# Kernel tuning notes

Measured on AMD Instinct MI355X. Metric: run time of the kernel, lower is better.

The kernel has to match this reference:

```python
import jax, jax.numpy as jnp
import numpy as np

NUM_HEADS = 8
HEAD_DIM = 64
EPS = 1e-4

def _act(x):
    # 1 + elu(x) == where(x > 0, x + 1, exp(x))
    return jnp.where(x > 0, x + 1.0, jnp.exp(x))

def setup_inputs() -> dict:
    key = jax.random.key(0)
    k1, k2, k3 = jax.random.split(key, 3)
    b, n, dim = 16, 4096, 512
    inner = NUM_HEADS * HEAD_DIM
    x = jax.random.normal(k1, (b, n, dim), dtype=jnp.float32)
    W_qkv = jax.random.normal(k2, (3 * inner, dim), dtype=jnp.float32) * (dim ** -0.5)
    W_out = jax.random.normal(k3, (dim, inner), dtype=jnp.float32) * (inner ** -0.5)
    b_out = jnp.zeros((dim,), dtype=jnp.float32)
    return {"x": x, "W_qkv": W_qkv, "W_out": W_out, "b_out": b_out}

def reference(x, W_qkv, W_out, b_out):
    b, n, dim = x.shape
    inner = NUM_HEADS * HEAD_DIM
    qkv = x @ W_qkv.T                                     # [b, n, 3*inner]
    q, k, v = jnp.split(qkv, 3, axis=-1)
    def to_heads(t):
        return t.reshape(b, n, NUM_HEADS, HEAD_DIM).transpose(0, 2, 1, 3)  # [b, h, n, d]
    q, k, v = to_heads(q), to_heads(k), to_heads(v)
    q = _act(q)
    k = _act(k)
    # kv = sum_n k_n (outer) v_n  -> [b, h, d, e]
    kv = jnp.einsum('bhnd,bhne->bhde', k, v)
    # denominator: q . sum_n k_n, clamped at eps
    k_sum = k.sum(axis=-2)                                # [b, h, d]
    z = 1.0 / jnp.maximum(jnp.einsum('bhnd,bhd->bhn', q, k_sum), EPS)
    out = jnp.einsum('bhnd,bhde,bhn->bhne', q, kv, z)     # [b, h, n, e]
    out = out.transpose(0, 2, 1, 3).reshape(b, n, inner)  # [b, n, h*d]
    return out @ W_out.T + b_out
```

## Files before the change

kernel.cpp:

```cpp
#include <hip/hip_runtime.h>


typedef unsigned short u16;
typedef u16 u16x4 __attribute__((ext_vector_type(4)));
typedef u16 u16x8 __attribute__((ext_vector_type(8)));
typedef __bf16 bf16x8 __attribute__((ext_vector_type(8)));
typedef float f32x4 __attribute__((ext_vector_type(4)));

__device__ __forceinline__ float bf2f(u16 x) {
    union { unsigned u; float f; } t; t.u = ((unsigned)x) << 16; return t.f;
}
__device__ __forceinline__ u16 f2bf(float f) {
    union { float f; unsigned u; } t; t.f = f;
    unsigned r = t.u + 0x7fffu + ((t.u >> 16) & 1u);
    return (u16)(r >> 16);
}
__device__ __forceinline__ float act_fn(float v) {
    return v > 0.0f ? v + 1.0f : __expf(v);
}
__device__ __forceinline__ void cvt8(const float* __restrict__ s, u16* __restrict__ d) {
    f32x4 lo = *(const f32x4*)s;
    f32x4 hi = *(const f32x4*)(s + 4);
    u16x8 o = { f2bf(lo[0]), f2bf(lo[1]), f2bf(lo[2]), f2bf(lo[3]),
                f2bf(hi[0]), f2bf(hi[1]), f2bf(hi[2]), f2bf(hi[3]) };
    *(u16x8*)d = o;
}
__device__ __forceinline__ void gld16(const u16* g, u16* l) {
    __builtin_amdgcn_global_load_lds(
        (__attribute__((address_space(1))) const void*)g,
        (__attribute__((address_space(3))) void*)l, 16, 0, 0);
}

__global__ __launch_bounds__(256) void convert_all(const float* __restrict__ x,
                                                   const float* __restrict__ Wqkv,
                                                   const float* __restrict__ Wout,
                                                   u16* __restrict__ xb,
                                                   u16* __restrict__ wq,
                                                   u16* __restrict__ wo,
                                                   float* __restrict__ kvg)
{
    size_t u = (size_t)blockIdx.x * 256 + threadIdx.x;
    if (u < 4194304ull) {
        cvt8(x + u * 8, xb + u * 8);
    } else if (u < 4292608ull) {
        u -= 4194304ull;
        const int drow = (int)(u >> 6);
        int srow;
        if (drow < 512) srow = drow;
        else {
            const int t = drow - 512, h = t >> 7, j = t & 127;
            srow = (j < 64) ? (512 + h * 64 + j) : (1024 + h * 64 + (j - 64));
        }
        cvt8(Wqkv + (size_t)srow * 512 + (u & 63) * 8, wq + u * 8);
    } else if (u < 4325376ull) {
        u -= 4292608ull; cvt8(Wout + u * 8, wo + u * 8);
    } else {
        u -= 4325376ull;
        f32x4 z = { 0.f, 0.f, 0.f, 0.f };
        *(f32x4*)&kvg[u * 8] = z;
        *(f32x4*)&kvg[u * 8 + 4] = z;
    }
}

__global__ __launch_bounds__(512, 4) void gemm_qkv(const u16* __restrict__ A,
                                                   const u16* __restrict__ Bw,
                                                   u16* __restrict__ Cq,
                                                   float* __restrict__ kvglob)
{
    __shared__ u16 SMF[16384];
    const int nt = blockIdx.x;
    const int mt = blockIdx.y;
    const size_t row0 = (size_t)mt * 128;
    const int col0 = nt * 128;
    const int tid = threadIdx.x, wave = tid >> 6, lane = tid & 63;
    const int frow = lane & 15, quad = lane >> 4;
    const int wr = (wave >> 1) * 32, wc = (wave & 1) * 64;

    f32x4 acc[2][4] = {};

    const int r0 = tid >> 2, c0 = (tid & 3) * 8;
    const u16* gA0 = A + (row0 + r0) * 512 + c0;
    const u16* gB0 = Bw + (size_t)(col0 + r0) * 512 + c0;

#define QKV_STAGE(buf, k0) do {                                   \
        u16* As_ = SMF + (buf) * 8192;                            \
        u16* Bs_ = As_ + 4096;                                    \
        gld16(gA0 + (k0), As_ + wave * 512);                      \
        gld16(gB0 + (k0), Bs_ + wave * 512);                      \
    } while (0)

    QKV_STAGE(0, 0);
    __syncthreads();
    int cur = 0;
    for (int t = 0; t < 16; ++t) {
        if (t < 15) QKV_STAGE(cur ^ 1, (t + 1) * 32);
        const u16* As_ = SMF + cur * 8192;
        const u16* Bs_ = As_ + 4096;
        bf16x8 af[2], bfr[4];
#pragma unroll
        for (int mi = 0; mi < 2; ++mi)
            af[mi] = *(const bf16x8*)&As_[(wr + mi * 16 + frow) * 32 + quad * 8];
#pragma unroll
        for (int ni = 0; ni < 4; ++ni)
            bfr[ni] = *(const bf16x8*)&Bs_[(wc + ni * 16 + frow) * 32 + quad * 8];
#pragma unroll
        for (int mi = 0; mi < 2; ++mi)
#pragma unroll
            for (int ni = 0; ni < 4; ++ni)
                acc[mi][ni] = __builtin_amdgcn_mfma_f32_16x16x32_bf16(af[mi], bfr[ni], acc[mi][ni], 0, 0, 0);
        __syncthreads();
        cur ^= 1;
    }
#undef QKV_STAGE

    if (col0 < 512) {
#pragma unroll
        for (int mi = 0; mi < 2; ++mi) {
#pragma unroll
            for (int ni = 0; ni < 4; ++ni) {
                const int c = col0 + wc + ni * 16 + frow;
                const size_t rbase = row0 + wr + mi * 16 + quad * 4;
#pragma unroll
                for (int reg = 0; reg < 4; ++reg)
                    Cq[(rbase + reg) * 512 + c] = f2bf(act_fn(acc[mi][ni][reg]));
            }
        }
        return;
    }

    u16* KT = SMF;
    u16* VT = SMF + 4608;
    for (int i = tid; i < 16 * 72; i += 512)
        VT[64 * 72 + i] = (i < 64) ? (u16)0x3F80 : (u16)0;

    const bool is_k = (wc == 0);
    f32x4 kvacc[5] = {};

#pragma unroll
    for (int half = 0; half < 2; ++half) {
        __syncthreads();
        if ((wave >> 2) == half) {
#pragma unroll
            for (int mi = 0; mi < 2; ++mi) {
                const int n0 = wr + mi * 16 + quad * 4 - half * 64;
#pragma unroll
                for (int ni = 0; ni < 4; ++ni) {
                    const int cl = wc + ni * 16 + frow;
                    u16x4 o2;
#pragma unroll
                    for (int reg = 0; reg < 4; ++reg) {
                        float v = acc[mi][ni][reg];
                        if (is_k) v = act_fn(v);
                        o2[reg] = f2bf(v);
                    }
                    if (is_k) *(u16x4*)&KT[cl * 72 + n0] = o2;
                    else      *(u16x4*)&VT[(cl - 64) * 72 + n0] = o2;
                }
            }
        }
        __syncthreads();
        if (wave < 4) {
#pragma unroll
            for (int c = 0; c < 2; ++c) {
                bf16x8 af2 = *(const bf16x8*)&KT[(wave * 16 + frow) * 72 + c * 32 + quad * 8];
#pragma unroll
                for (int et = 0; et < 5; ++et) {
                    bf16x8 bf2 = *(const bf16x8*)&VT[(et * 16 + frow) * 72 + c * 32 + quad * 8];
                    kvacc[et] = __builtin_amdgcn_mfma_f32_16x16x32_bf16(af2, bf2, kvacc[et], 0, 0, 0);
                }
            }
        }
    }

    if (wave < 4) {
        const int b = mt >> 5, h = nt - 4;
        float* dst = kvglob + (size_t)(b * 8 + h) * 5120;
#pragma unroll
        for (int et = 0; et < 5; ++et) {
            const int e = et * 16 + frow;
            if (e <= 64) {
#pragma unroll
                for (int reg = 0; reg < 4; ++reg) {
                    const int d = wave * 16 + quad * 4 + reg;
                    atomicAdd(&dst[d * 80 + e], kvacc[et][reg]);
                }
            }
        }
    }
}

__global__ __launch_bounds__(256) void make_P(const float* __restrict__ kvglob,
                                              const u16* __restrict__ wo,
                                              u16* __restrict__ P,
                                              u16* __restrict__ ksum)
{
    __shared__ u16 kvb[64 * 72];
    const int bh = blockIdx.x, b = bh >> 3, h = bh & 7;
    const int tid = threadIdx.x, wave = tid >> 6, lane = tid & 63;
    const int frow = lane & 15, quad = lane >> 4;
    const float* src = kvglob + (size_t)bh * 5120;

    for (int i = tid; i < 4096; i += 256)
        kvb[(i >> 6) * 72 + (i & 63)] = f2bf(src[(i >> 6) * 80 + (i & 63)]);
    if (tid < 64) ksum[bh * 64 + tid] = f2bf(src[tid * 80 + 64]);
    __syncthreads();

    f32x4 acc[8][4] = {};
    const int m0 = wave * 128;
#pragma unroll
    for (int k2 = 0; k2 < 2; ++k2) {
        bf16x8 bfr[4];
#pragma unroll
        for (int ni = 0; ni < 4; ++ni)
            bfr[ni] = *(const bf16x8*)&kvb[(ni * 16 + frow) * 72 + k2 * 32 + quad * 8];
#pragma unroll
        for (int mi = 0; mi < 8; ++mi) {
            bf16x8 af = *(const bf16x8*)&wo[(size_t)(m0 + mi * 16 + frow) * 512 + h * 64 + k2 * 32 + quad * 8];
#pragma unroll
            for (int ni = 0; ni < 4; ++ni)
                acc[mi][ni] = __builtin_amdgcn_mfma_f32_16x16x32_bf16(af, bfr[ni], acc[mi][ni], 0, 0, 0);
        }
    }

    u16* Pb = P + (size_t)b * 262144;
#pragma unroll
    for (int mi = 0; mi < 8; ++mi) {
#pragma unroll
        for (int ni = 0; ni < 4; ++ni) {
            const int d = ni * 16 + frow;
#pragma unroll
            for (int reg = 0; reg < 4; ++reg) {
                const int c = m0 + mi * 16 + quad * 4 + reg;
                Pb[(size_t)c * 512 + h * 64 + d] = f2bf(acc[mi][ni][reg]);
            }
        }
    }
}

__global__ __launch_bounds__(256) void apply_z(u16* __restrict__ qio,
                                               const u16* __restrict__ ksum)
{
    const int tid = threadIdx.x, wave = tid >> 6, lane = tid & 63;
    const int t0 = blockIdx.x * 64 + wave * 16;
    const int b = blockIdx.x >> 6;

    u16x8 k8 = *(const u16x8*)&ksum[b * 512 + lane * 8];
    float kf[8];
#pragma unroll
    for (int e = 0; e < 8; ++e) kf[e] = bf2f(k8[e]);

    for (int it = 0; it < 16; ++it) {
        u16* row = qio + (size_t)(t0 + it) * 512 + lane * 8;
        u16x8 q8 = *(const u16x8*)row;
        float den = 0.f;
#pragma unroll
        for (int e = 0; e < 8; ++e) den += bf2f(q8[e]) * kf[e];
        den += __shfl_xor(den, 1);
        den += __shfl_xor(den, 2);
        den += __shfl_xor(den, 4);
        const float z = 1.0f / fmaxf(den, 1e-4f);
        u16x8 o;
#pragma unroll
        for (int e = 0; e < 8; ++e) o[e] = f2bf(bf2f(q8[e]) * z);
        *(u16x8*)row = o;
    }
}

__global__ __launch_bounds__(512, 4) void gemm_final(const u16* __restrict__ A,
                                                     const u16* __restrict__ P,
                                                     float* __restrict__ C,
                                                     const float* __restrict__ bias)
{
    __shared__ u16 SMF[16384];
    const int nt = blockIdx.x;
    const int mt = blockIdx.y;
    const size_t row0 = (size_t)mt * 128;
    const int col0 = nt * 128;
    const u16* Bw = P + (size_t)(mt >> 5) * 262144;
    const int tid  = threadIdx.x;
    const int wave = tid >> 6, lane = tid & 63;
    const int wr = (wave >> 1) * 32, wc = (wave & 1) * 64;
    const int frow = lane & 15, quad = lane >> 4;

    f32x4 acc[2][4] = {};

    const int r0 = tid >> 2, c0 = (tid & 3) * 8;
    const u16* gA0 = A + (row0 + r0) * 512 + c0;
    const u16* gB0 = Bw + (size_t)(col0 + r0) * 512 + c0;

#define OUT_STAGE(buf, k0) do {                                   \
        u16* As_ = SMF + (buf) * 8192;                            \
        u16* Bs_ = As_ + 4096;                                    \
        gld16(gA0 + (k0), As_ + wave * 512);                      \
        gld16(gB0 + (k0), Bs_ + wave * 512);                      \
    } while (0)

    OUT_STAGE(0, 0);
    __syncthreads();
    int cur = 0;
    for (int t = 0; t < 16; ++t) {
        if (t < 15) OUT_STAGE(cur ^ 1, (t + 1) * 32);
        const u16* As_ = SMF + cur * 8192;
        const u16* Bs_ = As_ + 4096;
        bf16x8 af[2], bfr[4];
#pragma unroll
        for (int mi = 0; mi < 2; ++mi)
            af[mi] = *(const bf16x8*)&As_[(wr + mi * 16 + frow) * 32 + quad * 8];
#pragma unroll
        for (int ni = 0; ni < 4; ++ni)
            bfr[ni] = *(const bf16x8*)&Bs_[(wc + ni * 16 + frow) * 32 + quad * 8];
#pragma unroll
        for (int mi = 0; mi < 2; ++mi)
#pragma unroll
            for (int ni = 0; ni < 4; ++ni)
                acc[mi][ni] = __builtin_amdgcn_mfma_f32_16x16x32_bf16(af[mi], bfr[ni], acc[mi][ni], 0, 0, 0);
        __syncthreads();
        cur ^= 1;
    }
#undef OUT_STAGE

#pragma unroll
    for (int mi = 0; mi < 2; ++mi) {
#pragma unroll
        for (int ni = 0; ni < 4; ++ni) {
            const int c = col0 + wc + ni * 16 + frow;
            const float bv = bias[c];
            const size_t rbase = row0 + wr + mi * 16 + quad * 4;
#pragma unroll
            for (int reg = 0; reg < 4; ++reg)
                C[(rbase + reg) * 512 + c] = acc[mi][ni][reg] + bv;
        }
    }
}

extern "C" void kernel_launch(void* const* d_in, const int* in_sizes, int n_in,
                              void* d_out, int out_size, void* d_ws, size_t ws_size,
                              hipStream_t stream)
{
    const float* x    = (const float*)d_in[0];
    const float* Wqkv = (const float*)d_in[1];
    const float* Wout = (const float*)d_in[2];
    const float* bout = (const float*)d_in[3];
    float* out = (float*)d_out;
    char* ws = (char*)d_ws;

    u16*   wq_bf  = (u16*)ws;
    u16*   wo_bf  = (u16*)(ws + 1572864ull);
    u16*   wsq    = (u16*)(ws + 2097152ull);
    u16*   xb     = (u16*)(ws + 69206016ull);
    u16*   P      = xb;
    float* kvglob = (float*)(ws + 136314880ull);
    u16*   ksum   = (u16*)(ws + 138936320ull);

    convert_all<<<17216, 256, 0, stream>>>(x, Wqkv, Wout, xb, wq_bf, wo_bf, kvglob);
    gemm_qkv<<<dim3(12, 512), 512, 0, stream>>>(xb, wq_bf, wsq, kvglob);
    make_P<<<128, 256, 0, stream>>>(kvglob, wo_bf, P, ksum);
    apply_z<<<1024, 256, 0, stream>>>(wsq, ksum);
    gemm_final<<<dim3(4, 512), 512, 0, stream>>>(wsq, P, out, bout);
}
```

Before: 481.4 us.

## Fuse per-head normalization into output GEMM and widen K tiles with swizzled LDS

Removes the separate apply_z pass. The output GEMM now computes each row's per-head denominator with an extra MFMA against ksum, since each 64-wide K tile is exactly one head. It then scales the partial products by 1/max(den, eps) before adding them into the output accumulator. Both GEMMs also move from 32-wide to 64-wide K tiles with XOR-swizzled LDS, which halves the loop iterations and barriers and should reduce bank conflicts. The cost is double the shared memory per block, which can lower occupancy, plus extra MFMA and per-tile scaling work in the final GEMM.

```diff
diff --git a/kernel.cpp b/kernel.cpp
--- a/kernel.cpp
+++ b/kernel.cpp
@@ -67,7 +67,7 @@
                                                    u16* __restrict__ Cq,
                                                    float* __restrict__ kvglob)
 {
-    __shared__ u16 SMF[16384];
+    __shared__ u16 SMF[32768];
     const int nt = blockIdx.x;
     const int mt = blockIdx.y;
     const size_t row0 = (size_t)mt * 128;
@@ -78,36 +78,50 @@
 
     f32x4 acc[2][4] = {};
 
-    const int r0 = tid >> 2, c0 = (tid & 3) * 8;
-    const u16* gA0 = A + (row0 + r0) * 512 + c0;
-    const u16* gB0 = Bw + (size_t)(col0 + r0) * 512 + c0;
+    const int ch0 = wave * 64 + lane, ch1 = 512 + ch0;
+    const int ar0 = ch0 >> 3, ac0 = ((ch0 & 7) ^ (ar0 & 7)) * 8;
+    const int ar1 = ch1 >> 3, ac1 = ((ch1 & 7) ^ (ar1 & 7)) * 8;
+    const u16* gA0 = A + (row0 + ar0) * 512 + ac0;
+    const u16* gA1 = A + (row0 + ar1) * 512 + ac1;
+    const u16* gB0 = Bw + (size_t)(col0 + ar0) * 512 + ac0;
+    const u16* gB1 = Bw + (size_t)(col0 + ar1) * 512 + ac1;
 
 #define QKV_STAGE(buf, k0) do {                                   \
-        u16* As_ = SMF + (buf) * 8192;                            \
-        u16* Bs_ = As_ + 4096;                                    \
+        u16* As_ = SMF + (buf) * 16384;                           \
+        u16* Bs_ = As_ + 8192;                                    \
         gld16(gA0 + (k0), As_ + wave * 512);                      \
+        gld16(gA1 + (k0), As_ + 4096 + wave * 512);               \
         gld16(gB0 + (k0), Bs_ + wave * 512);                      \
+        gld16(gB1 + (k0), Bs_ + 4096 + wave * 512);               \
     } while (0)
 
     QKV_STAGE(0, 0);
     __syncthreads();
     int cur = 0;
-    for (int t = 0; t < 16; ++t) {
-        if (t < 15) QKV_STAGE(cur ^ 1, (t + 1) * 32);
-        const u16* As_ = SMF + cur * 8192;
-        const u16* Bs_ = As_ + 4096;
-        bf16x8 af[2], bfr[4];
-#pragma unroll
-        for (int mi = 0; mi < 2; ++mi)
-            af[mi] = *(const bf16x8*)&As_[(wr + mi * 16 + frow) * 32 + quad * 8];
-#pragma unroll
-        for (int ni = 0; ni < 4; ++ni)
-            bfr[ni] = *(const bf16x8*)&Bs_[(wc + ni * 16 + frow) * 32 + quad * 8];
-#pragma unroll
-        for (int mi = 0; mi < 2; ++mi)
-#pragma unroll
-            for (int ni = 0; ni < 4; ++ni)
-                acc[mi][ni] = __builtin_amdgcn_mfma_f32_16x16x32_bf16(af[mi], bfr[ni], acc[mi][ni], 0, 0, 0);
+    for (int t = 0; t < 8; ++t) {
+        if (t < 7) QKV_STAGE(cur ^ 1, (t + 1) * 64);
+        const u16* As_ = SMF + cur * 16384;
+        const u16* Bs_ = As_ + 8192;
+#pragma unroll
+        for (int kk = 0; kk < 2; ++kk) {
+            const int cbase = kk * 32 + quad * 8;
+            bf16x8 af[2], bfr[4];
+#pragma unroll
+            for (int mi = 0; mi < 2; ++mi) {
+                const int r = wr + mi * 16 + frow;
+                af[mi] = *(const bf16x8*)&As_[r * 64 + (cbase ^ ((r & 7) * 8))];
+            }
+#pragma unroll
+            for (int ni = 0; ni < 4; ++ni) {
+                const int r = wc + ni * 16 + frow;
+                bfr[ni] = *(const bf16x8*)&Bs_[r * 64 + (cbase ^ ((r & 7) * 8))];
+            }
+#pragma unroll
+            for (int mi = 0; mi < 2; ++mi)
+#pragma unroll
+                for (int ni = 0; ni < 4; ++ni)
+                    acc[mi][ni] = __builtin_amdgcn_mfma_f32_16x16x32_bf16(af[mi], bfr[ni], acc[mi][ni], 0, 0, 0);
+        }
         __syncthreads();
         cur ^= 1;
     }
@@ -237,83 +251,86 @@
     }
 }
 
-__global__ __launch_bounds__(256) void apply_z(u16* __restrict__ qio,
-                                               const u16* __restrict__ ksum)
-{
-    const int tid = threadIdx.x, wave = tid >> 6, lane = tid & 63;
-    const int t0 = blockIdx.x * 64 + wave * 16;
-    const int b = blockIdx.x >> 6;
-
-    u16x8 k8 = *(const u16x8*)&ksum[b * 512 + lane * 8];
-    float kf[8];
-#pragma unroll
-    for (int e = 0; e < 8; ++e) kf[e] = bf2f(k8[e]);
-
-    for (int it = 0; it < 16; ++it) {
-        u16* row = qio + (size_t)(t0 + it) * 512 + lane * 8;
-        u16x8 q8 = *(const u16x8*)row;
-        float den = 0.f;
-#pragma unroll
-        for (int e = 0; e < 8; ++e) den += bf2f(q8[e]) * kf[e];
-        den += __shfl_xor(den, 1);
-        den += __shfl_xor(den, 2);
-        den += __shfl_xor(den, 4);
-        const float z = 1.0f / fmaxf(den, 1e-4f);
-        u16x8 o;
-#pragma unroll
-        for (int e = 0; e < 8; ++e) o[e] = f2bf(bf2f(q8[e]) * z);
-        *(u16x8*)row = o;
-    }
-}
-
 __global__ __launch_bounds__(512, 4) void gemm_final(const u16* __restrict__ A,
                                                      const u16* __restrict__ P,
                                                      float* __restrict__ C,
-                                                     const float* __restrict__ bias)
-{
-    __shared__ u16 SMF[16384];
+                                                     const float* __restrict__ bias,
+                                                     const u16* __restrict__ ksum)
+{
+    __shared__ u16 SMF[32768];
+    __shared__ u16 ksumL[512];
     const int nt = blockIdx.x;
     const int mt = blockIdx.y;
     const size_t row0 = (size_t)mt * 128;
     const int col0 = nt * 128;
-    const u16* Bw = P + (size_t)(mt >> 5) * 262144;
+    const int bb = mt >> 5;
+    const u16* Bw = P + (size_t)bb * 262144;
     const int tid  = threadIdx.x;
     const int wave = tid >> 6, lane = tid & 63;
     const int wr = (wave >> 1) * 32, wc = (wave & 1) * 64;
     const int frow = lane & 15, quad = lane >> 4;
 
-    f32x4 acc[2][4] = {};
-
-    const int r0 = tid >> 2, c0 = (tid & 3) * 8;
-    const u16* gA0 = A + (row0 + r0) * 512 + c0;
-    const u16* gB0 = Bw + (size_t)(col0 + r0) * 512 + c0;
+    f32x4 oacc[2][4] = {};
+
+    const int ch0 = wave * 64 + lane, ch1 = 512 + ch0;
+    const int ar0 = ch0 >> 3, ac0 = ((ch0 & 7) ^ (ar0 & 7)) * 8;
+    const int ar1 = ch1 >> 3, ac1 = ((ch1 & 7) ^ (ar1 & 7)) * 8;
+    const u16* gA0 = A + (row0 + ar0) * 512 + ac0;
+    const u16* gA1 = A + (row0 + ar1) * 512 + ac1;
+    const u16* gB0 = Bw + (size_t)(col0 + ar0) * 512 + ac0;
+    const u16* gB1 = Bw + (size_t)(col0 + ar1) * 512 + ac1;
 
 #define OUT_STAGE(buf, k0) do {                                   \
-        u16* As_ = SMF + (buf) * 8192;                            \
-        u16* Bs_ = As_ + 4096;                                    \
+        u16* As_ = SMF + (buf) * 16384;                           \
+        u16* Bs_ = As_ + 8192;                                    \
         gld16(gA0 + (k0), As_ + wave * 512);                      \
+        gld16(gA1 + (k0), As_ + 4096 + wave * 512);               \
         gld16(gB0 + (k0), Bs_ + wave * 512);                      \
+        gld16(gB1 + (k0), Bs_ + 4096 + wave * 512);               \
     } while (0)
 
     OUT_STAGE(0, 0);
+    if (tid < 64) *(u16x8*)&ksumL[tid * 8] = *(const u16x8*)&ksum[bb * 512 + tid * 8];
     __syncthreads();
     int cur = 0;
-    for (int t = 0; t < 16; ++t) {
-        if (t < 15) OUT_STAGE(cur ^ 1, (t + 1) * 32);
-        const u16* As_ = SMF + cur * 8192;
-        const u16* Bs_ = As_ + 4096;
-        bf16x8 af[2], bfr[4];
+    for (int t = 0; t < 8; ++t) {
+        if (t < 7) OUT_STAGE(cur ^ 1, (t + 1) * 64);
+        const u16* As_ = SMF + cur * 16384;
+        const u16* Bs_ = As_ + 8192;
+        f32x4 sacc[2][4] = {};
+        f32x4 dacc[2] = {};
+#pragma unroll
+        for (int kk = 0; kk < 2; ++kk) {
+            const int cbase = kk * 32 + quad * 8;
+            bf16x8 af[2], bfr[4];
+#pragma unroll
+            for (int mi = 0; mi < 2; ++mi) {
+                const int r = wr + mi * 16 + frow;
+                af[mi] = *(const bf16x8*)&As_[r * 64 + (cbase ^ ((r & 7) * 8))];
+            }
+#pragma unroll
+            for (int ni = 0; ni < 4; ++ni) {
+                const int r = wc + ni * 16 + frow;
+                bfr[ni] = *(const bf16x8*)&Bs_[r * 64 + (cbase ^ ((r & 7) * 8))];
+            }
+            bf16x8 kf = *(const bf16x8*)&ksumL[t * 64 + kk * 32 + quad * 8];
+#pragma unroll
+            for (int mi = 0; mi < 2; ++mi) {
+                dacc[mi] = __builtin_amdgcn_mfma_f32_16x16x32_bf16(af[mi], kf, dacc[mi], 0, 0, 0);
+#pragma unroll
+                for (int ni = 0; ni < 4; ++ni)
+                    sacc[mi][ni] = __builtin_amdgcn_mfma_f32_16x16x32_bf16(af[mi], bfr[ni], sacc[mi][ni], 0, 0, 0);
+            }
+        }
 #pragma unroll
         for (int mi = 0; mi < 2; ++mi)
-            af[mi] = *(const bf16x8*)&As_[(wr + mi * 16 + frow) * 32 + quad * 8];
-#pragma unroll
-        for (int ni = 0; ni < 4; ++ni)
-            bfr[ni] = *(const bf16x8*)&Bs_[(wc + ni * 16 + frow) * 32 + quad * 8];
-#pragma unroll
-        for (int mi = 0; mi < 2; ++mi)
-#pragma unroll
-            for (int ni = 0; ni < 4; ++ni)
-                acc[mi][ni] = __builtin_amdgcn_mfma_f32_16x16x32_bf16(af[mi], bfr[ni], acc[mi][ni], 0, 0, 0);
+#pragma unroll
+            for (int reg = 0; reg < 4; ++reg) {
+                const float z = 1.0f / fmaxf(dacc[mi][reg], 1e-4f);
+#pragma unroll
+                for (int ni = 0; ni < 4; ++ni)
+                    oacc[mi][ni][reg] += sacc[mi][ni][reg] * z;
+            }
         __syncthreads();
         cur ^= 1;
     }
@@ -328,7 +345,7 @@
             const size_t rbase = row0 + wr + mi * 16 + quad * 4;
 #pragma unroll
             for (int reg = 0; reg < 4; ++reg)
-                C[(rbase + reg) * 512 + c] = acc[mi][ni][reg] + bv;
+                C[(rbase + reg) * 512 + c] = oacc[mi][ni][reg] + bv;
         }
     }
 }
@@ -355,6 +372,5 @@
     convert_all<<<17216, 256, 0, stream>>>(x, Wqkv, Wout, xb, wq_bf, wo_bf, kvglob);
     gemm_qkv<<<dim3(12, 512), 512, 0, stream>>>(xb, wq_bf, wsq, kvglob);
     make_P<<<128, 256, 0, stream>>>(kvglob, wo_bf, P, ksum);
-    apply_z<<<1024, 256, 0, stream>>>(wsq, ksum);
-    gemm_final<<<dim3(4, 512), 512, 0, stream>>>(wsq, P, out, bout);
-}
+    gemm_final<<<dim3(4, 512), 512, 0, stream>>>(wsq, P, out, bout, ksum);
+}
```

Result: faster. 448.7 us (-6.8%).
